# Optimization experiments

Measured on AMD Instinct MI355X. Metric: run time of the kernel, lower is better.

Reference implementation:

```python
import jax, jax.numpy as jnp
import numpy as np


def setup_inputs() -> dict:
    key = jax.random.key(0)
    k1, k2 = jax.random.split(key)
    B, N, M, D = 8, 8192, 8192, 3
    pred_seq = jax.random.normal(k1, (B, N, D), dtype=jnp.float32)
    tgt_output = jax.random.normal(k2, (B, M, D), dtype=jnp.float32)
    return {"pred_seq": pred_seq, "tgt_output": tgt_output}


def reference(pred_seq, tgt_output):
    # Euclidean pairwise distances [B, N, M] (== torch.cdist with p=2).
    # The torch module computes both cdist(pred,tgt) and cdist(tgt,pred);
    # they are transposes, so we compute one matrix and min over both axes.
    sq_p = jnp.sum(pred_seq * pred_seq, axis=-1)      # [B, N]
    sq_t = jnp.sum(tgt_output * tgt_output, axis=-1)  # [B, M]
    cross = jnp.einsum('bnd,bmd->bnm', pred_seq, tgt_output)  # [B, N, M]
    d2 = sq_p[:, :, None] + sq_t[:, None, :] - 2.0 * cross
    d = jnp.sqrt(jnp.maximum(d2, 0.0))
    min_pred_to_true = jnp.min(d, axis=2)   # [B, N]
    min_true_to_pred = jnp.min(d, axis=1)   # [B, M]
    chamfer = (jnp.mean(min_pred_to_true, axis=1) + jnp.mean(min_true_to_pred, axis=1)) / 2.0
    return chamfer  # [B]
```

## Files before the change

### kernel.cpp

```cpp
#include <hip/hip_runtime.h>
#include <math.h>

#define BB 8
#define NPTS 8192
#define NSIDE (BB * NPTS)

#define BLOCK 256
#define WARPS 4
#define ROWSB (32 * WARPS)
#define TCHUNK 2048
#define NTILES (TCHUNK / 32)

#define INF_KEY 0x7F7F7F7F

typedef short bf16x8 __attribute__((ext_vector_type(8)));
typedef float f32x16 __attribute__((ext_vector_type(16)));

__device__ __forceinline__ int enc_key(float v) {
    int b = __float_as_int(v);
    return b >= 0 ? b : (b ^ 0x7fffffff);
}
__device__ __forceinline__ float dec_key(int k) {
    int b = k >= 0 ? k : (k ^ 0x7fffffff);
    return __int_as_float(b);
}
__device__ __forceinline__ unsigned short f2bf(float f) {
    unsigned u = __float_as_uint(f);
    return (unsigned short)((u + 0x7FFFu + ((u >> 16) & 1u)) >> 16);
}
__device__ __forceinline__ float bfhi(float f, unsigned short* bits) {
    unsigned short h = f2bf(f);
    *bits = h;
    return __uint_as_float(((unsigned)h) << 16);
}
__device__ __forceinline__ void pack16(unsigned short* dst, const unsigned short* s) {
    uint4* d4 = (uint4*)dst;
    uint4 w0 = {(unsigned)s[0] | ((unsigned)s[1] << 16),
                (unsigned)s[2] | ((unsigned)s[3] << 16),
                (unsigned)s[4] | ((unsigned)s[5] << 16),
                (unsigned)s[6] | ((unsigned)s[7] << 16)};
    uint4 w1 = {(unsigned)s[8] | ((unsigned)s[9] << 16),
                (unsigned)s[10] | ((unsigned)s[11] << 16),
                (unsigned)s[12] | ((unsigned)s[13] << 16),
                (unsigned)s[14] | ((unsigned)s[15] << 16)};
    d4[0] = w0; d4[1] = w1;
}

__global__ __launch_bounds__(BLOCK) void chamfer_pack(
        const float* __restrict__ pred, const float* __restrict__ tgt,
        unsigned short* __restrict__ pA, unsigned short* __restrict__ pB,
        int* __restrict__ rk, int* __restrict__ ck, float* __restrict__ out) {
    int i = blockIdx.x * BLOCK + threadIdx.x;
    const unsigned short one = 0x3F80;
    {
        float x = pred[(size_t)i * 3 + 0], y = pred[(size_t)i * 3 + 1],
              z = pred[(size_t)i * 3 + 2];
        float wq = fmaf(x, x, fmaf(y, y, z * z));
        float ax = -2.0f * x, ay = -2.0f * y, az = -2.0f * z;
        unsigned short hx, hy, hz, hw;
        float fhx = bfhi(ax, &hx), fhy = bfhi(ay, &hy), fhz = bfhi(az, &hz);
        float fhw = bfhi(wq, &hw);
        unsigned short lx = f2bf(ax - fhx), ly = f2bf(ay - fhy),
                       lz = f2bf(az - fhz), lw = f2bf(wq - fhw);
        unsigned short s[16] = {hx, hx, lx, hy, hy, ly, hz, hz, lz,
                                hw, lw, one, one, 0, 0, 0};
        pack16(pA + (size_t)i * 16, s);
    }
    {
        float x = tgt[(size_t)i * 3 + 0], y = tgt[(size_t)i * 3 + 1],
              z = tgt[(size_t)i * 3 + 2];
        float tw = fmaf(x, x, fmaf(y, y, z * z));
        unsigned short hx, hy, hz, hw;
        float fhx = bfhi(x, &hx), fhy = bfhi(y, &hy), fhz = bfhi(z, &hz);
        float fhw = bfhi(tw, &hw);
        unsigned short lx = f2bf(x - fhx), ly = f2bf(y - fhy),
                       lz = f2bf(z - fhz), lw = f2bf(tw - fhw);
        unsigned short s[16] = {hx, lx, hx, hy, ly, hy, hz, lz, hz,
                                one, one, hw, lw, 0, 0, 0};
        pack16(pB + (size_t)i * 16, s);
    }
    rk[i] = INF_KEY;
    ck[i] = INF_KEY;
    if (i < BB) out[i] = 0.0f;
}

__global__ __launch_bounds__(BLOCK) void chamfer_mfma(
        const unsigned short* __restrict__ pA, const unsigned short* __restrict__ pB,
        int* __restrict__ rk, int* __restrict__ ck) {
    const int b = blockIdx.z;
    const int tb0 = blockIdx.x * TCHUNK;
    const int rb0 = blockIdx.y * ROWSB;
    const int wave = threadIdx.x >> 6;
    const int lane = threadIdx.x & 63;
    const int lp = lane & 31;
    const int kh = lane >> 5;

    __shared__ float colslice[WARPS][TCHUNK];

    const bf16x8* Ap = (const bf16x8*)pA;
    const bf16x8* Bp = (const bf16x8*)pB;
    const bf16x8 afrag = Ap[(size_t)(b * NPTS + rb0 + wave * 32 + lp) * 2 + kh];

    f32x16 zerov;
    #pragma unroll
    for (int k = 0; k < 16; ++k) zerov[k] = 0.0f;
    asm("" : "+v"(zerov));

    float rmin[16];
    #pragma unroll
    for (int k = 0; k < 16; ++k) rmin[k] = INFINITY;

    const bf16x8* bp = Bp + (size_t)(b * NPTS + tb0 + lp) * 2 + kh;

    #pragma unroll 4
    for (int tile = 0; tile < NTILES; ++tile) {
        const bf16x8 bfrag = bp[tile * 64];
        f32x16 d = __builtin_amdgcn_mfma_f32_32x32x16_bf16(
            afrag, bfrag, zerov, 0, 0, 0);
        asm("" : "+v"(d));
        #pragma unroll
        for (int k = 0; k < 16; ++k) rmin[k] = fminf(rmin[k], d[k]);
        float c0 = fminf(fminf(d[0], d[1]), d[2]);
        float c1 = fminf(fminf(d[3], d[4]), d[5]);
        float c2 = fminf(fminf(d[6], d[7]), d[8]);
        float c3 = fminf(fminf(d[9], d[10]), d[11]);
        float c4 = fminf(fminf(d[12], d[13]), d[14]);
        float cp = fminf(fminf(fminf(c0, c1), fminf(c2, c3)),
                         fminf(c4, d[15]));
        cp = fminf(cp, __shfl_xor(cp, 32));
        if (lane < 32) colslice[wave][tile * 32 + lane] = cp;
    }
    __syncthreads();

    for (int j = threadIdx.x; j < TCHUNK; j += BLOCK) {
        float m = fminf(fminf(colslice[0][j], colslice[1][j]),
                        fminf(colslice[2][j], colslice[3][j]));
        atomicMin(&ck[(size_t)b * NPTS + tb0 + j], enc_key(m));
    }

    #pragma unroll
    for (int k = 0; k < 16; ++k) {
        #pragma unroll
        for (int off = 1; off <= 16; off <<= 1)
            rmin[k] = fminf(rmin[k], __shfl_xor(rmin[k], off));
    }
    if (lp == 0) {
        #pragma unroll
        for (int k = 0; k < 16; ++k) {
            int row = (k & 3) + 8 * (k >> 2) + 4 * kh;
            atomicMin(&rk[(size_t)b * NPTS + rb0 + wave * 32 + row],
                      enc_key(rmin[k]));
        }
    }
}

#define FSLICE 32
__global__ __launch_bounds__(BLOCK) void chamfer_finalize(
        const int* __restrict__ rk, const int* __restrict__ ck,
        float* __restrict__ out) {
    const int b = blockIdx.x / FSLICE;
    const int s = blockIdx.x % FSLICE;
    const int t = threadIdx.x;
    const int i = b * NPTS + s * (NPTS / FSLICE) + t;
    float v = sqrtf(fmaxf(dec_key(rk[i]), 0.0f)) +
              sqrtf(fmaxf(dec_key(ck[i]), 0.0f));
    __shared__ float red[BLOCK];
    red[t] = v * (0.5f / (float)NPTS);
    __syncthreads();
    for (int off = BLOCK / 2; off > 0; off >>= 1) {
        if (t < off) red[t] += red[t + off];
        __syncthreads();
    }
    if (t == 0) atomicAdd(&out[b], red[0]);
}

extern "C" void kernel_launch(void* const* d_in, const int* in_sizes, int n_in,
                              void* d_out, int out_size, void* d_ws, size_t ws_size,
                              hipStream_t stream) {
    const float* pred = (const float*)d_in[0];
    const float* tgtp = (const float*)d_in[1];
    float* out = (float*)d_out;

    char* ws = (char*)d_ws;
    unsigned short* pA = (unsigned short*)ws;
    unsigned short* pB = (unsigned short*)(ws + (size_t)NSIDE * 32);
    int* rk = (int*)(ws + (size_t)2 * NSIDE * 32);
    int* ck = rk + NSIDE;

    chamfer_pack<<<NSIDE / BLOCK, BLOCK, 0, stream>>>(pred, tgtp, pA, pB, rk, ck, out);

    chamfer_mfma<<<dim3(NPTS / TCHUNK, NPTS / ROWSB, BB), BLOCK, 0, stream>>>(
        pA, pB, rk, ck);

    chamfer_finalize<<<BB * FSLICE, BLOCK, 0, stream>>>(rk, ck, out);
}
```

Before: 156.0 us.

## Compute row and column minima in separate passes and fuse finalize into last block

The column-min reduction (per-tile shuffle, shared-memory slice, and column atomics) is removed. The matrix is instead computed twice, once per direction, with A and B swapped via the grid z index, so each pass does only cheap per-register row minima. The separate finalize kernel is replaced by a last-block-done counter that performs the final sqrt/mean reduction, saving a launch. The cost is twice the MFMA work and a serial single-block final reduction over all points. The -2 scaling also moves from the pred packing to the tgt packing so the swapped product stays symmetric.

```diff
diff --git a/kernel.cpp b/kernel.cpp
--- a/kernel.cpp
+++ b/kernel.cpp
@@ -6,10 +6,12 @@
 #define NSIDE (BB * NPTS)
 
 #define BLOCK 256
-#define WARPS 4
-#define ROWSB (32 * WARPS)
-#define TCHUNK 2048
+#define TCH 4
+#define TCHUNK (NPTS / TCH)
 #define NTILES (TCHUNK / 32)
+#define ROWSB 128
+#define NRB (NPTS / ROWSB)
+#define TOTALBLK (TCH * NRB * 16)
 
 #define INF_KEY 0x7F7F7F7F
 
@@ -49,19 +51,19 @@
 __global__ __launch_bounds__(BLOCK) void chamfer_pack(
         const float* __restrict__ pred, const float* __restrict__ tgt,
         unsigned short* __restrict__ pA, unsigned short* __restrict__ pB,
-        int* __restrict__ rk, int* __restrict__ ck, float* __restrict__ out) {
+        int* __restrict__ rk, int* __restrict__ ck,
+        float* __restrict__ out, int* __restrict__ done) {
     int i = blockIdx.x * BLOCK + threadIdx.x;
     const unsigned short one = 0x3F80;
     {
         float x = pred[(size_t)i * 3 + 0], y = pred[(size_t)i * 3 + 1],
               z = pred[(size_t)i * 3 + 2];
-        float wq = fmaf(x, x, fmaf(y, y, z * z));
-        float ax = -2.0f * x, ay = -2.0f * y, az = -2.0f * z;
+        float w = fmaf(x, x, fmaf(y, y, z * z));
         unsigned short hx, hy, hz, hw;
-        float fhx = bfhi(ax, &hx), fhy = bfhi(ay, &hy), fhz = bfhi(az, &hz);
-        float fhw = bfhi(wq, &hw);
-        unsigned short lx = f2bf(ax - fhx), ly = f2bf(ay - fhy),
-                       lz = f2bf(az - fhz), lw = f2bf(wq - fhw);
+        float fx = bfhi(x, &hx), fy = bfhi(y, &hy), fz = bfhi(z, &hz);
+        float fw = bfhi(w, &hw);
+        unsigned short lx = f2bf(x - fx), ly = f2bf(y - fy),
+                       lz = f2bf(z - fz), lw = f2bf(w - fw);
         unsigned short s[16] = {hx, hx, lx, hy, hy, ly, hz, hz, lz,
                                 hw, lw, one, one, 0, 0, 0};
         pack16(pA + (size_t)i * 16, s);
@@ -69,12 +71,13 @@
     {
         float x = tgt[(size_t)i * 3 + 0], y = tgt[(size_t)i * 3 + 1],
               z = tgt[(size_t)i * 3 + 2];
-        float tw = fmaf(x, x, fmaf(y, y, z * z));
+        float w = fmaf(x, x, fmaf(y, y, z * z));
+        float ux = -2.0f * x, uy = -2.0f * y, uz = -2.0f * z;
         unsigned short hx, hy, hz, hw;
-        float fhx = bfhi(x, &hx), fhy = bfhi(y, &hy), fhz = bfhi(z, &hz);
-        float fhw = bfhi(tw, &hw);
-        unsigned short lx = f2bf(x - fhx), ly = f2bf(y - fhy),
-                       lz = f2bf(z - fhz), lw = f2bf(tw - fhw);
+        float fx = bfhi(ux, &hx), fy = bfhi(uy, &hy), fz = bfhi(uz, &hz);
+        float fw = bfhi(w, &hw);
+        unsigned short lx = f2bf(ux - fx), ly = f2bf(uy - fy),
+                       lz = f2bf(uz - fz), lw = f2bf(w - fw);
         unsigned short s[16] = {hx, lx, hx, hy, ly, hy, hz, lz, hz,
                                 one, one, hw, lw, 0, 0, 0};
         pack16(pB + (size_t)i * 16, s);
@@ -82,12 +85,15 @@
     rk[i] = INF_KEY;
     ck[i] = INF_KEY;
     if (i < BB) out[i] = 0.0f;
+    if (i == 0) *done = 0;
 }
 
-__global__ __launch_bounds__(BLOCK) void chamfer_mfma(
+__global__ __launch_bounds__(BLOCK) void chamfer_mm(
         const unsigned short* __restrict__ pA, const unsigned short* __restrict__ pB,
-        int* __restrict__ rk, int* __restrict__ ck) {
-    const int b = blockIdx.z;
+        int* __restrict__ rk, int* __restrict__ ck,
+        float* __restrict__ out, int* __restrict__ done) {
+    const int dir = blockIdx.z >> 3;
+    const int b = blockIdx.z & 7;
     const int tb0 = blockIdx.x * TCHUNK;
     const int rb0 = blockIdx.y * ROWSB;
     const int wave = threadIdx.x >> 6;
@@ -95,11 +101,12 @@
     const int lp = lane & 31;
     const int kh = lane >> 5;
 
-    __shared__ float colslice[WARPS][TCHUNK];
+    const bf16x8* Aarr = (const bf16x8*)(dir ? pB : pA);
+    const bf16x8* Barr = (const bf16x8*)(dir ? pA : pB);
+    int* keys = dir ? ck : rk;
 
-    const bf16x8* Ap = (const bf16x8*)pA;
-    const bf16x8* Bp = (const bf16x8*)pB;
-    const bf16x8 afrag = Ap[(size_t)(b * NPTS + rb0 + wave * 32 + lp) * 2 + kh];
+    const bf16x8 afrag = Aarr[(size_t)(b * NPTS + rb0 + wave * 32 + lp) * 2 + kh];
+    const bf16x8* bp = Barr + (size_t)(b * NPTS + tb0 + lp) * 2 + kh;
 
     f32x16 zerov;
     #pragma unroll
@@ -110,9 +117,7 @@
     #pragma unroll
     for (int k = 0; k < 16; ++k) rmin[k] = INFINITY;
 
-    const bf16x8* bp = Bp + (size_t)(b * NPTS + tb0 + lp) * 2 + kh;
-
-    #pragma unroll 4
+    #pragma unroll 2
     for (int tile = 0; tile < NTILES; ++tile) {
         const bf16x8 bfrag = bp[tile * 64];
         f32x16 d = __builtin_amdgcn_mfma_f32_32x32x16_bf16(
@@ -120,22 +125,6 @@
         asm("" : "+v"(d));
         #pragma unroll
         for (int k = 0; k < 16; ++k) rmin[k] = fminf(rmin[k], d[k]);
-        float c0 = fminf(fminf(d[0], d[1]), d[2]);
-        float c1 = fminf(fminf(d[3], d[4]), d[5]);
-        float c2 = fminf(fminf(d[6], d[7]), d[8]);
-        float c3 = fminf(fminf(d[9], d[10]), d[11]);
-        float c4 = fminf(fminf(d[12], d[13]), d[14]);
-        float cp = fminf(fminf(fminf(c0, c1), fminf(c2, c3)),
-                         fminf(c4, d[15]));
-        cp = fminf(cp, __shfl_xor(cp, 32));
-        if (lane < 32) colslice[wave][tile * 32 + lane] = cp;
-    }
-    __syncthreads();
-
-    for (int j = threadIdx.x; j < TCHUNK; j += BLOCK) {
-        float m = fminf(fminf(colslice[0][j], colslice[1][j]),
-                        fminf(colslice[2][j], colslice[3][j]));
-        atomicMin(&ck[(size_t)b * NPTS + tb0 + j], enc_key(m));
     }
 
     #pragma unroll
@@ -148,30 +137,41 @@
         #pragma unroll
         for (int k = 0; k < 16; ++k) {
             int row = (k & 3) + 8 * (k >> 2) + 4 * kh;
-            atomicMin(&rk[(size_t)b * NPTS + rb0 + wave * 32 + row],
+            atomicMin(&keys[(size_t)b * NPTS + rb0 + wave * 32 + row],
                       enc_key(rmin[k]));
         }
     }
-}
 
-#define FSLICE 32
-__global__ __launch_bounds__(BLOCK) void chamfer_finalize(
-        const int* __restrict__ rk, const int* __restrict__ ck,
-        float* __restrict__ out) {
-    const int b = blockIdx.x / FSLICE;
-    const int s = blockIdx.x % FSLICE;
-    const int t = threadIdx.x;
-    const int i = b * NPTS + s * (NPTS / FSLICE) + t;
-    float v = sqrtf(fmaxf(dec_key(rk[i]), 0.0f)) +
-              sqrtf(fmaxf(dec_key(ck[i]), 0.0f));
+    __threadfence();
+    __syncthreads();
+    __shared__ int lastflag;
+    if (threadIdx.x == 0) {
+        int old = __hip_atomic_fetch_add(done, 1, __ATOMIC_ACQ_REL,
+                                         __HIP_MEMORY_SCOPE_AGENT);
+        lastflag = (old == TOTALBLK - 1);
+    }
+    __syncthreads();
+    if (!lastflag) return;
+
     __shared__ float red[BLOCK];
-    red[t] = v * (0.5f / (float)NPTS);
-    __syncthreads();
-    for (int off = BLOCK / 2; off > 0; off >>= 1) {
-        if (t < off) red[t] += red[t + off];
+    for (int bb = 0; bb < BB; ++bb) {
+        float s = 0.0f;
+        for (int j = threadIdx.x; j < NPTS; j += BLOCK) {
+            int kr = __hip_atomic_load(&rk[(size_t)bb * NPTS + j],
+                                       __ATOMIC_RELAXED, __HIP_MEMORY_SCOPE_AGENT);
+            int kc = __hip_atomic_load(&ck[(size_t)bb * NPTS + j],
+                                       __ATOMIC_RELAXED, __HIP_MEMORY_SCOPE_AGENT);
+            s += sqrtf(fmaxf(dec_key(kr), 0.0f)) + sqrtf(fmaxf(dec_key(kc), 0.0f));
+        }
+        red[threadIdx.x] = s;
+        __syncthreads();
+        for (int off = BLOCK / 2; off > 0; off >>= 1) {
+            if (threadIdx.x < off) red[threadIdx.x] += red[threadIdx.x + off];
+            __syncthreads();
+        }
+        if (threadIdx.x == 0) out[bb] = red[0] * (0.5f / (float)NPTS);
         __syncthreads();
     }
-    if (t == 0) atomicAdd(&out[b], red[0]);
 }
 
 extern "C" void kernel_launch(void* const* d_in, const int* in_sizes, int n_in,
@@ -186,11 +186,10 @@
     unsigned short* pB = (unsigned short*)(ws + (size_t)NSIDE * 32);
     int* rk = (int*)(ws + (size_t)2 * NSIDE * 32);
     int* ck = rk + NSIDE;
+    int* done = ck + NSIDE;
 
-    chamfer_pack<<<NSIDE / BLOCK, BLOCK, 0, stream>>>(pred, tgtp, pA, pB, rk, ck, out);
+    chamfer_pack<<<NSIDE / BLOCK, BLOCK, 0, stream>>>(pred, tgtp, pA, pB,
+                                                      rk, ck, out, done);
 
-    chamfer_mfma<<<dim3(NPTS / TCHUNK, NPTS / ROWSB, BB), BLOCK, 0, stream>>>(
-        pA, pB, rk, ck);
-
-    chamfer_finalize<<<BB * FSLICE, BLOCK, 0, stream>>>(rk, ck, out);
+    chamfer_mm<<<dim3(TCH, NRB, 16), BLOCK, 0, stream>>>(pA, pB, rk, ck, out, done);
 }
```

Result: slower. 518.3 us (+232.2%).
